# Optimization experiments

Hardware: AMD Instinct MI355X
Metric: run time of the kernel (lower is better)

The kernel has to match this reference:

```python
import jax, jax.numpy as jnp
import numpy as np

NUM_GRAPHS = 64
NEG_SLOPE = 0.1


def gcn_conv(x, src, dst, W, b, num_nodes):
    h = x @ W  # [N, out]
    ones = jnp.ones(src.shape[0], dtype=x.dtype)
    deg = jax.ops.segment_sum(ones, dst, num_segments=num_nodes) + 1.0  # +1 self-loop
    dinv = jax.lax.rsqrt(deg)  # deg >= 1 always
    coef = dinv[src] * dinv[dst]  # [E]
    agg = jax.ops.segment_sum(h[src] * coef[:, None], dst, num_segments=num_nodes)
    # self-loop contribution: dinv[i]^2 * h[i]
    out = agg + h * (dinv * dinv)[:, None] + b
    return out


def leaky_relu(x):
    return jnp.where(x >= 0, x, NEG_SLOPE * x)


def global_mean_pool(x, batch, num_graphs):
    s = jax.ops.segment_sum(x, batch, num_segments=num_graphs)
    cnt = jax.ops.segment_sum(jnp.ones(x.shape[0], dtype=x.dtype), batch, num_segments=num_graphs)
    return s / jnp.maximum(cnt, 1.0)[:, None]


def setup_inputs() -> dict:
    key = jax.random.key(0)
    ks = jax.random.split(key, 10)
    N, E, D_IN, D_H, D_OUT, C = 50000, 600000, 128, 128, 128, 16
    x = jax.random.normal(ks[0], (N, D_IN), dtype=jnp.float32)
    edge_index = jax.random.randint(ks[1], (2, E), 0, N, dtype=jnp.int32)
    batch = jnp.sort(jax.random.randint(ks[2], (N,), 0, NUM_GRAPHS, dtype=jnp.int32))
    def glorot(k, shape):
        lim = np.sqrt(6.0 / (shape[0] + shape[1]))
        return jax.random.uniform(k, shape, jnp.float32, -lim, lim)
    W1 = glorot(ks[3], (D_IN, D_H))
    b1 = jnp.zeros((D_H,), jnp.float32)
    W2 = glorot(ks[4], (D_H, D_OUT))
    b2 = jnp.zeros((D_OUT,), jnp.float32)
    Wl = glorot(ks[5], (D_OUT, C))
    bl = jnp.zeros((C,), jnp.float32)
    return {"x": x, "edge_index": edge_index, "batch": batch,
            "W1": W1, "b1": b1, "W2": W2, "b2": b2, "Wl": Wl, "bl": bl}


def reference(x, edge_index, batch, W1, b1, W2, b2, Wl, bl):
    N = x.shape[0]
    src, dst = edge_index[0], edge_index[1]
    h = gcn_conv(x, src, dst, W1, b1, N)
    h = leaky_relu(h)
    h = gcn_conv(h, src, dst, W2, b2, N)
    h = leaky_relu(h)
    g = global_mean_pool(h, batch, NUM_GRAPHS)  # [G, D_OUT]
    # dropout p=0.2 is identity in eval mode
    return g @ Wl + bl
```

## Files before the change

kernel.cpp:

```cpp
#include <hip/hip_runtime.h>

#define D 128
#define NG 64
#define NC 16
#define NEG 0.1f

typedef __attribute__((ext_vector_type(8))) short bf16x8;
typedef __attribute__((ext_vector_type(4))) float f32x4;

__device__ __forceinline__ float bf2f(unsigned int u16) {
    union { unsigned int i; float f; } c;
    c.i = u16 << 16;
    return c.f;
}
__device__ __forceinline__ unsigned short f2bf(float f) {
    union { float f; unsigned int i; } c;
    c.f = f;
    unsigned int i = c.i;
    unsigned int r = (i + 0x7FFFu + ((i >> 16) & 1u)) >> 16;
    return (unsigned short)r;
}

__global__ void prep_misc_kernel(const float* __restrict__ W1, unsigned short* __restrict__ Wf1,
                                 const float* __restrict__ W2, unsigned short* __restrict__ Wf2,
                                 float* __restrict__ pooled,
                                 const int* __restrict__ dst, int* __restrict__ deg, int E) {
    int b = blockIdx.x;
    if (b < 16) {
        const float* W = (b < 8) ? W1 : W2;
        unsigned short* Wf = (b < 8) ? Wf1 : Wf2;
        int fid = (b & 7) * 256 + threadIdx.x;
        int m = fid & 15;
        int quad = (fid >> 4) & 3;
        int kc = (fid >> 6) & 3;
        int t = fid >> 8;
        int n = t * 16 + m;
        int k0 = kc * 32 + quad * 8;
        unsigned short r[8];
#pragma unroll
        for (int j = 0; j < 8; j++) r[j] = f2bf(W[(k0 + j) * 128 + n]);
        uint4 v;
        v.x = (unsigned int)r[0] | ((unsigned int)r[1] << 16);
        v.y = (unsigned int)r[2] | ((unsigned int)r[3] << 16);
        v.z = (unsigned int)r[4] | ((unsigned int)r[5] << 16);
        v.w = (unsigned int)r[6] | ((unsigned int)r[7] << 16);
        ((uint4*)Wf)[fid] = v;
    } else if (b < 48) {
        pooled[(b - 16) * 256 + threadIdx.x] = 0.f;
    } else {
        int e = (b - 48) * 256 + threadIdx.x;
        if (e < E) atomicAdd(&deg[dst[e]], 1);
    }
}

__global__ void scan_block_kernel(const int* __restrict__ deg, int* __restrict__ scan1,
                                  int* __restrict__ blocksum, float* __restrict__ dinv, int N) {
    __shared__ int sm[256];
    int tid = threadIdx.x;
    int i = blockIdx.x * 256 + tid;
    int v = (i < N) ? deg[i] : 0;
    if (i < N) dinv[i] = 1.0f / sqrtf((float)v + 1.0f);
    sm[tid] = v;
    __syncthreads();
    for (int off = 1; off < 256; off <<= 1) {
        int t = (tid >= off) ? sm[tid - off] : 0;
        __syncthreads();
        sm[tid] += t;
        __syncthreads();
    }
    if (i < N) scan1[i] = sm[tid];
    if (tid == 255) blocksum[blockIdx.x] = sm[255];
}

__global__ void finalize_ptr_kernel(const int* __restrict__ deg, const int* __restrict__ scan1,
                                    const int* __restrict__ blocksum, int* __restrict__ ptr,
                                    int* __restrict__ fill, int nb, int N, int E) {
    __shared__ int sm[256];
    int tid = threadIdx.x;
    int v = (tid < nb) ? blocksum[tid] : 0;
    sm[tid] = v;
    __syncthreads();
    for (int off = 1; off < 256; off <<= 1) {
        int t = (tid >= off) ? sm[tid - off] : 0;
        __syncthreads();
        sm[tid] += t;
        __syncthreads();
    }
    int blockoff = (blockIdx.x > 0) ? sm[blockIdx.x - 1] : 0;
    int i = blockIdx.x * 256 + tid;
    if (i < N) {
        ptr[i] = scan1[i] - deg[i] + blockoff;
        fill[i] = 0;
        if (i == N - 1) ptr[N] = E;
    }
}

__global__ void scatter_kernel(const int* __restrict__ src, const int* __restrict__ dst,
                               const int* __restrict__ ptr, int* __restrict__ fill,
                               const float* __restrict__ dinv,
                               int2* __restrict__ csr_edge, int E) {
    int e = blockIdx.x * blockDim.x + threadIdx.x;
    if (e < E) {
        int d = dst[e];
        int s = src[e];
        int pos = ptr[d] + atomicAdd(&fill[d], 1);
        float coef = dinv[s] * dinv[d];
        csr_edge[pos] = make_int2(s, __float_as_int(coef));
    }
}

template <bool AF32>
__global__ __launch_bounds__(256) void gemm_mfma_kernel(const void* __restrict__ Ap,
                                                        const uint4* __restrict__ Wf,
                                                        unsigned int* __restrict__ C, int N) {
    __shared__ uint4 Ws[2048];
    int tid = threadIdx.x;
    int w = tid >> 6, lane = tid & 63;
    int quad = lane >> 4, m = lane & 15;
    int rowstart = blockIdx.x * 64;

#pragma unroll
    for (int i = 0; i < 8; i++) Ws[tid + 256 * i] = Wf[tid + 256 * i];

    int arow = rowstart + 16 * w + m;
    bool valid = arow < N;
    bf16x8 af[4];
    if (AF32) {
        const float* Ag = (const float*)Ap;
#pragma unroll
        for (int kc = 0; kc < 4; kc++) {
            float4 f0 = make_float4(0.f, 0.f, 0.f, 0.f), f1 = f0;
            if (valid) {
                const float4* p = (const float4*)(Ag + (size_t)arow * 128 + kc * 32 + quad * 8);
                f0 = p[0];
                f1 = p[1];
            }
            bf16x8 a;
            a[0] = (short)f2bf(f0.x); a[1] = (short)f2bf(f0.y);
            a[2] = (short)f2bf(f0.z); a[3] = (short)f2bf(f0.w);
            a[4] = (short)f2bf(f1.x); a[5] = (short)f2bf(f1.y);
            a[6] = (short)f2bf(f1.z); a[7] = (short)f2bf(f1.w);
            af[kc] = a;
        }
    } else {
        const unsigned short* Ag = (const unsigned short*)Ap;
#pragma unroll
        for (int kc = 0; kc < 4; kc++) {
            bf16x8 a;
#pragma unroll
            for (int j = 0; j < 8; j++) a[j] = 0;
            if (valid) a = *(const bf16x8*)(Ag + (size_t)arow * 128 + kc * 32 + quad * 8);
            af[kc] = a;
        }
    }
    __syncthreads();

    f32x4 acc[8];
#pragma unroll
    for (int t = 0; t < 8; t++) acc[t] = (f32x4){0.f, 0.f, 0.f, 0.f};

#pragma unroll
    for (int t = 0; t < 8; t++) {
#pragma unroll
        for (int kc = 0; kc < 4; kc++) {
            bf16x8 bh = *(const bf16x8*)&Ws[(((t * 4 + kc) * 4 + quad) * 16 + m)];
            acc[t] = __builtin_amdgcn_mfma_f32_16x16x32_bf16(af[kc], bh, acc[t], 0, 0, 0);
        }
    }

#pragma unroll
    for (int t = 0; t < 8; t++) {
#pragma unroll
        for (int r = 0; r < 4; r++) {
            int row = rowstart + 16 * w + quad * 4 + r;
            unsigned int us = f2bf(acc[t][r]);
            unsigned int other = (unsigned int)__shfl_xor((int)us, 1);
            if (((m & 1) == 0) && row < N)
                C[(size_t)row * 64 + t * 8 + (m >> 1)] = us | (other << 16);
        }
    }
}

__global__ void combine_kernel(const uint4* __restrict__ h4, const int* __restrict__ ptr,
                               const int2* __restrict__ csr_edge,
                               const float* __restrict__ dinv, const float* __restrict__ b,
                               uint4* __restrict__ out4, int N) {
    __shared__ int2 smeta[4][64];
    int wave = threadIdx.x >> 6;
    int lane = threadIdx.x & 63;
    int i = blockIdx.x * 4 + wave;
    if (i >= N) return;
    int q = lane >> 4;
    int l16 = lane & 15;

    int lo = ptr[i], hi = ptr[i + 1];
    int deg = hi - lo;

    float a0 = 0.f, a1 = 0.f, a2 = 0.f, a3 = 0.f, a4 = 0.f, a5 = 0.f, a6 = 0.f, a7 = 0.f;

    for (int base = 0; base < deg; base += 64) {
        int cnt = min(64, deg - base);
        if (lane < cnt) smeta[wave][lane] = csr_edge[lo + base + lane];
        int jj = q;
        for (; jj + 4 < cnt; jj += 8) {
            int2 e0 = smeta[wave][jj];
            int2 e1 = smeta[wave][jj + 4];
            float c0 = __int_as_float(e0.y);
            float c1 = __int_as_float(e1.y);
            uint4 v0 = h4[(size_t)e0.x * 16 + l16];
            uint4 v1 = h4[(size_t)e1.x * 16 + l16];
            a0 += bf2f(v0.x & 0xffffu) * c0; a1 += bf2f(v0.x >> 16) * c0;
            a2 += bf2f(v0.y & 0xffffu) * c0; a3 += bf2f(v0.y >> 16) * c0;
            a4 += bf2f(v0.z & 0xffffu) * c0; a5 += bf2f(v0.z >> 16) * c0;
            a6 += bf2f(v0.w & 0xffffu) * c0; a7 += bf2f(v0.w >> 16) * c0;
            a0 += bf2f(v1.x & 0xffffu) * c1; a1 += bf2f(v1.x >> 16) * c1;
            a2 += bf2f(v1.y & 0xffffu) * c1; a3 += bf2f(v1.y >> 16) * c1;
            a4 += bf2f(v1.z & 0xffffu) * c1; a5 += bf2f(v1.z >> 16) * c1;
            a6 += bf2f(v1.w & 0xffffu) * c1; a7 += bf2f(v1.w >> 16) * c1;
        }
        if (jj < cnt) {
            int2 e0 = smeta[wave][jj];
            float c0 = __int_as_float(e0.y);
            uint4 v0 = h4[(size_t)e0.x * 16 + l16];
            a0 += bf2f(v0.x & 0xffffu) * c0; a1 += bf2f(v0.x >> 16) * c0;
            a2 += bf2f(v0.y & 0xffffu) * c0; a3 += bf2f(v0.y >> 16) * c0;
            a4 += bf2f(v0.z & 0xffffu) * c0; a5 += bf2f(v0.z >> 16) * c0;
            a6 += bf2f(v0.w & 0xffffu) * c0; a7 += bf2f(v0.w >> 16) * c0;
        }
    }
    a0 += __shfl_xor(a0, 16); a0 += __shfl_xor(a0, 32);
    a1 += __shfl_xor(a1, 16); a1 += __shfl_xor(a1, 32);
    a2 += __shfl_xor(a2, 16); a2 += __shfl_xor(a2, 32);
    a3 += __shfl_xor(a3, 16); a3 += __shfl_xor(a3, 32);
    a4 += __shfl_xor(a4, 16); a4 += __shfl_xor(a4, 32);
    a5 += __shfl_xor(a5, 16); a5 += __shfl_xor(a5, 32);
    a6 += __shfl_xor(a6, 16); a6 += __shfl_xor(a6, 32);
    a7 += __shfl_xor(a7, 16); a7 += __shfl_xor(a7, 32);

    float di = dinv[i];
    uint4 sv = h4[(size_t)i * 16 + l16];
    float4 bv0 = ((const float4*)b)[l16 * 2];
    float4 bv1 = ((const float4*)b)[l16 * 2 + 1];
    float dd = di * di;
    float v0 = a0 + bf2f(sv.x & 0xffffu) * dd + bv0.x;
    float v1 = a1 + bf2f(sv.x >> 16) * dd + bv0.y;
    float v2 = a2 + bf2f(sv.y & 0xffffu) * dd + bv0.z;
    float v3 = a3 + bf2f(sv.y >> 16) * dd + bv0.w;
    float v4 = a4 + bf2f(sv.z & 0xffffu) * dd + bv1.x;
    float v5 = a5 + bf2f(sv.z >> 16) * dd + bv1.y;
    float v6 = a6 + bf2f(sv.w & 0xffffu) * dd + bv1.z;
    float v7 = a7 + bf2f(sv.w >> 16) * dd + bv1.w;
    v0 = (v0 >= 0.f) ? v0 : NEG * v0;
    v1 = (v1 >= 0.f) ? v1 : NEG * v1;
    v2 = (v2 >= 0.f) ? v2 : NEG * v2;
    v3 = (v3 >= 0.f) ? v3 : NEG * v3;
    v4 = (v4 >= 0.f) ? v4 : NEG * v4;
    v5 = (v5 >= 0.f) ? v5 : NEG * v5;
    v6 = (v6 >= 0.f) ? v6 : NEG * v6;
    v7 = (v7 >= 0.f) ? v7 : NEG * v7;
    if (q == 0) {
        uint4 pv;
        pv.x = (unsigned int)f2bf(v0) | ((unsigned int)f2bf(v1) << 16);
        pv.y = (unsigned int)f2bf(v2) | ((unsigned int)f2bf(v3) << 16);
        pv.z = (unsigned int)f2bf(v4) | ((unsigned int)f2bf(v5) << 16);
        pv.w = (unsigned int)f2bf(v6) | ((unsigned int)f2bf(v7) << 16);
        out4[(size_t)i * 16 + l16] = pv;
    }
}

#define PROWS 128
__global__ void pool_accum_kernel(const unsigned int* __restrict__ a2,
                                  const int* __restrict__ batch,
                                  float* __restrict__ pooled, int N) {
    int wave = threadIdx.x >> 6;
    int lane = threadIdx.x & 63;
    int start = blockIdx.x * PROWS;
    int end = start + PROWS;
    if (end > N) end = N;
    float s0 = 0.f, s1 = 0.f;
    int curg = -1;
    for (int r = start + wave; r < end; r += 4) {
        int g = batch[r];
        if (g != curg) {
            if (curg >= 0) {
                atomicAdd(&pooled[curg * D + 2 * lane], s0);
                atomicAdd(&pooled[curg * D + 2 * lane + 1], s1);
            }
            curg = g;
            s0 = 0.f;
            s1 = 0.f;
        }
        unsigned int v = a2[(size_t)r * 64 + lane];
        s0 += bf2f(v & 0xffffu);
        s1 += bf2f(v >> 16);
    }
    if (curg >= 0) {
        atomicAdd(&pooled[curg * D + 2 * lane], s0);
        atomicAdd(&pooled[curg * D + 2 * lane + 1], s1);
    }
}

__global__ void final_kernel(const float* __restrict__ pooled, const int* __restrict__ batch,
                             const float* __restrict__ Wl, const float* __restrict__ bl,
                             float* __restrict__ out, int N) {
    int t = blockIdx.x * blockDim.x + threadIdx.x;
    if (t >= NG * NC) return;
    int g = t >> 4, c = t & 15;
    int l = 0, h = N;
    while (l < h) { int m = (l + h) >> 1; if (batch[m] < g) l = m + 1; else h = m; }
    int lo = l;
    h = N;
    while (l < h) { int m = (l + h) >> 1; if (batch[m] < g + 1) l = m + 1; else h = m; }
    int cnt = l - lo;
    float inv = 1.0f / (float)(cnt > 0 ? cnt : 1);
    float dot = 0.f;
    for (int k = 0; k < D; k++) dot += pooled[g * D + k] * Wl[k * NC + c];
    out[t] = dot * inv + bl[c];
}

extern "C" void kernel_launch(void* const* d_in, const int* in_sizes, int n_in,
                              void* d_out, int out_size, void* d_ws, size_t ws_size,
                              hipStream_t stream) {
    const float* x = (const float*)d_in[0];
    const int* ei = (const int*)d_in[1];
    const int* batch = (const int*)d_in[2];
    const float* W1 = (const float*)d_in[3];
    const float* b1 = (const float*)d_in[4];
    const float* W2 = (const float*)d_in[5];
    const float* b2 = (const float*)d_in[6];
    const float* Wlin = (const float*)d_in[7];
    const float* bl = (const float*)d_in[8];
    float* out = (float*)d_out;

    int N = in_sizes[0] / D;
    int E = in_sizes[1] / 2;
    const int* src = ei;
    const int* dst = ei + E;

    float* ws = (float*)d_ws;
    size_t o = 0;
    unsigned int* bufA = (unsigned int*)(ws + o); o += (size_t)N * 64;
    unsigned int* bufB = (unsigned int*)(ws + o); o += (size_t)N * 64;
    int* deg = (int*)(ws + o);      o += N;
    int* fill = (int*)(ws + o);     o += N;
    float* dinv = ws + o;           o += N;
    int* scan1 = (int*)(ws + o);    o += N;
    int* blocksum = (int*)(ws + o); o += 256;
    int* csr_ptr = (int*)(ws + o);  o += (N + 4);
    int2* csr_edge = (int2*)(ws + o); o += (size_t)2 * E;
    float* pooled = ws + o;         o += NG * D;
    unsigned short* Wf1 = (unsigned short*)(ws + o); o += 8192;
    unsigned short* Wf2 = (unsigned short*)(ws + o); o += 8192;

    hipMemsetAsync(deg, 0, (size_t)N * sizeof(int), stream);

    int tb = 256;
    int nscan = (N + 255) / 256;
    prep_misc_kernel<<<48 + (E + 255) / 256, 256, 0, stream>>>(W1, Wf1, W2, Wf2, pooled,
                                                               dst, deg, E);
    scan_block_kernel<<<nscan, 256, 0, stream>>>(deg, scan1, blocksum, dinv, N);
    finalize_ptr_kernel<<<nscan, 256, 0, stream>>>(deg, scan1, blocksum, csr_ptr, fill,
                                                   nscan, N, E);
    scatter_kernel<<<(E + tb - 1) / tb, tb, 0, stream>>>(src, dst, csr_ptr, fill, dinv,
                                                         csr_edge, E);

    int gblocks = (N + 63) / 64;
    int cblocks = (N + 3) / 4;
    gemm_mfma_kernel<true><<<gblocks, 256, 0, stream>>>(x, (const uint4*)Wf1,
                                                        (unsigned int*)bufA, N);
    combine_kernel<<<cblocks, 256, 0, stream>>>((const uint4*)bufA, csr_ptr, csr_edge,
                                                dinv, b1, (uint4*)bufB, N);
    gemm_mfma_kernel<false><<<gblocks, 256, 0, stream>>>(bufB, (const uint4*)Wf2,
                                                         (unsigned int*)bufA, N);
    combine_kernel<<<cblocks, 256, 0, stream>>>((const uint4*)bufA, csr_ptr, csr_edge,
                                                dinv, b2, (uint4*)bufB, N);
    pool_accum_kernel<<<(N + PROWS - 1) / PROWS, 256, 0, stream>>>(bufB, batch, pooled, N);
    final_kernel<<<(NG * NC + tb - 1) / tb, tb, 0, stream>>>(pooled, batch, Wlin, bl, out, N);
}
```

Measured before the change: 251.7 us.

## Map one node per 16-lane quarter-wave in GCN combine kernel

The combine kernel now assigns four nodes per wave, one per 16-lane group, instead of one node per wave with its edges split across the four quarters. The cross-quarter shuffle reduction goes away, and the edge metadata for the wave's four-node range is staged jointly into shared memory. Each quarter loops over its own node's edges, with four gathers in flight per iteration, and the grid shrinks fourfold. Degree imbalance among the four nodes in a wave can now leave lanes idle, since quarters with short edge lists wait on the longest one.

Measured after the change: 243.6 us. 1.03x faster.

```diff
diff --git a/kernel.cpp b/kernel.cpp
--- a/kernel.cpp
+++ b/kernel.cpp
@@ -181,66 +181,77 @@
     }
 }
 
-__global__ void combine_kernel(const uint4* __restrict__ h4, const int* __restrict__ ptr,
-                               const int2* __restrict__ csr_edge,
-                               const float* __restrict__ dinv, const float* __restrict__ b,
-                               uint4* __restrict__ out4, int N) {
+#define ACC8(v, c)                                                         \
+    a0 += bf2f((v).x & 0xffffu) * (c); a1 += bf2f((v).x >> 16) * (c);      \
+    a2 += bf2f((v).y & 0xffffu) * (c); a3 += bf2f((v).y >> 16) * (c);      \
+    a4 += bf2f((v).z & 0xffffu) * (c); a5 += bf2f((v).z >> 16) * (c);      \
+    a6 += bf2f((v).w & 0xffffu) * (c); a7 += bf2f((v).w >> 16) * (c);
+
+__global__ __launch_bounds__(256) void combine_kernel(const uint4* __restrict__ h4,
+                                                      const int* __restrict__ ptr,
+                                                      const int2* __restrict__ csr_edge,
+                                                      const float* __restrict__ dinv,
+                                                      const float* __restrict__ b,
+                                                      uint4* __restrict__ out4, int N) {
     __shared__ int2 smeta[4][64];
     int wave = threadIdx.x >> 6;
     int lane = threadIdx.x & 63;
-    int i = blockIdx.x * 4 + wave;
-    if (i >= N) return;
     int q = lane >> 4;
     int l16 = lane & 15;
-
-    int lo = ptr[i], hi = ptr[i + 1];
-    int deg = hi - lo;
+    int nb = blockIdx.x * 16 + wave * 4;
+    if (nb >= N) return;
+    int node = nb + q;
+    bool valid = node < N;
+
+    int wlo = ptr[nb];
+    int whi = ptr[min(nb + 4, N)];
+    int lo = valid ? ptr[node] : 0;
+    int hi = valid ? ptr[node + 1] : 0;
+
+    float di = valid ? dinv[node] : 0.f;
+    uint4 sv = valid ? h4[(size_t)node * 16 + l16] : make_uint4(0u, 0u, 0u, 0u);
+    float4 bv0 = ((const float4*)b)[l16 * 2];
+    float4 bv1 = ((const float4*)b)[l16 * 2 + 1];
 
     float a0 = 0.f, a1 = 0.f, a2 = 0.f, a3 = 0.f, a4 = 0.f, a5 = 0.f, a6 = 0.f, a7 = 0.f;
 
-    for (int base = 0; base < deg; base += 64) {
-        int cnt = min(64, deg - base);
-        if (lane < cnt) smeta[wave][lane] = csr_edge[lo + base + lane];
-        int jj = q;
-        for (; jj + 4 < cnt; jj += 8) {
-            int2 e0 = smeta[wave][jj];
-            int2 e1 = smeta[wave][jj + 4];
+#pragma unroll 1
+    for (int base = wlo; base < whi; base += 64) {
+        if (base + lane < whi) smeta[wave][lane] = csr_edge[base + lane];
+        int s = max(lo, base);
+        int e = min(hi, base + 64);
+        int j = s;
+#pragma unroll 1
+        for (; j + 3 < e; j += 4) {
+            int k = j - base;
+            int2 e0 = smeta[wave][k];
+            int2 e1 = smeta[wave][k + 1];
+            int2 e2 = smeta[wave][k + 2];
+            int2 e3 = smeta[wave][k + 3];
+            uint4 v0 = h4[(size_t)e0.x * 16 + l16];
+            uint4 v1 = h4[(size_t)e1.x * 16 + l16];
+            uint4 v2 = h4[(size_t)e2.x * 16 + l16];
+            uint4 v3 = h4[(size_t)e3.x * 16 + l16];
             float c0 = __int_as_float(e0.y);
             float c1 = __int_as_float(e1.y);
+            float c2 = __int_as_float(e2.y);
+            float c3 = __int_as_float(e3.y);
+            ACC8(v0, c0)
+            ACC8(v1, c1)
+            ACC8(v2, c2)
+            ACC8(v3, c3)
+        }
+#pragma unroll 1
+        for (; j < e; j++) {
+            int k = j - base;
+            int2 e0 = smeta[wave][k];
             uint4 v0 = h4[(size_t)e0.x * 16 + l16];
-            uint4 v1 = h4[(size_t)e1.x * 16 + l16];
-            a0 += bf2f(v0.x & 0xffffu) * c0; a1 += bf2f(v0.x >> 16) * c0;
-            a2 += bf2f(v0.y & 0xffffu) * c0; a3 += bf2f(v0.y >> 16) * c0;
-            a4 += bf2f(v0.z & 0xffffu) * c0; a5 += bf2f(v0.z >> 16) * c0;
-            a6 += bf2f(v0.w & 0xffffu) * c0; a7 += bf2f(v0.w >> 16) * c0;
-            a0 += bf2f(v1.x & 0xffffu) * c1; a1 += bf2f(v1.x >> 16) * c1;
-            a2 += bf2f(v1.y & 0xffffu) * c1; a3 += bf2f(v1.y >> 16) * c1;
-            a4 += bf2f(v1.z & 0xffffu) * c1; a5 += bf2f(v1.z >> 16) * c1;
-            a6 += bf2f(v1.w & 0xffffu) * c1; a7 += bf2f(v1.w >> 16) * c1;
-        }
-        if (jj < cnt) {
-            int2 e0 = smeta[wave][jj];
             float c0 = __int_as_float(e0.y);
-            uint4 v0 = h4[(size_t)e0.x * 16 + l16];
-            a0 += bf2f(v0.x & 0xffffu) * c0; a1 += bf2f(v0.x >> 16) * c0;
-            a2 += bf2f(v0.y & 0xffffu) * c0; a3 += bf2f(v0.y >> 16) * c0;
-            a4 += bf2f(v0.z & 0xffffu) * c0; a5 += bf2f(v0.z >> 16) * c0;
-            a6 += bf2f(v0.w & 0xffffu) * c0; a7 += bf2f(v0.w >> 16) * c0;
-        }
-    }
-    a0 += __shfl_xor(a0, 16); a0 += __shfl_xor(a0, 32);
-    a1 += __shfl_xor(a1, 16); a1 += __shfl_xor(a1, 32);
-    a2 += __shfl_xor(a2, 16); a2 += __shfl_xor(a2, 32);
-    a3 += __shfl_xor(a3, 16); a3 += __shfl_xor(a3, 32);
-    a4 += __shfl_xor(a4, 16); a4 += __shfl_xor(a4, 32);
-    a5 += __shfl_xor(a5, 16); a5 += __shfl_xor(a5, 32);
-    a6 += __shfl_xor(a6, 16); a6 += __shfl_xor(a6, 32);
-    a7 += __shfl_xor(a7, 16); a7 += __shfl_xor(a7, 32);
-
-    float di = dinv[i];
-    uint4 sv = h4[(size_t)i * 16 + l16];
-    float4 bv0 = ((const float4*)b)[l16 * 2];
-    float4 bv1 = ((const float4*)b)[l16 * 2 + 1];
+            ACC8(v0, c0)
+        }
+    }
+
+    if (!valid) return;
     float dd = di * di;
     float v0 = a0 + bf2f(sv.x & 0xffffu) * dd + bv0.x;
     float v1 = a1 + bf2f(sv.x >> 16) * dd + bv0.y;
@@ -258,14 +269,12 @@
     v5 = (v5 >= 0.f) ? v5 : NEG * v5;
     v6 = (v6 >= 0.f) ? v6 : NEG * v6;
     v7 = (v7 >= 0.f) ? v7 : NEG * v7;
-    if (q == 0) {
-        uint4 pv;
-        pv.x = (unsigned int)f2bf(v0) | ((unsigned int)f2bf(v1) << 16);
-        pv.y = (unsigned int)f2bf(v2) | ((unsigned int)f2bf(v3) << 16);
-        pv.z = (unsigned int)f2bf(v4) | ((unsigned int)f2bf(v5) << 16);
-        pv.w = (unsigned int)f2bf(v6) | ((unsigned int)f2bf(v7) << 16);
-        out4[(size_t)i * 16 + l16] = pv;
-    }
+    uint4 pv;
+    pv.x = (unsigned int)f2bf(v0) | ((unsigned int)f2bf(v1) << 16);
+    pv.y = (unsigned int)f2bf(v2) | ((unsigned int)f2bf(v3) << 16);
+    pv.z = (unsigned int)f2bf(v4) | ((unsigned int)f2bf(v5) << 16);
+    pv.w = (unsigned int)f2bf(v6) | ((unsigned int)f2bf(v7) << 16);
+    out4[(size_t)node * 16 + l16] = pv;
 }
 
 #define PROWS 128
@@ -365,7 +374,7 @@
                                                          csr_edge, E);
 
     int gblocks = (N + 63) / 64;
-    int cblocks = (N + 3) / 4;
+    int cblocks = (N + 15) / 16;
     gemm_mfma_kernel<true><<<gblocks, 256, 0, stream>>>(x, (const uint4*)Wf1,
                                                         (unsigned int*)bufA, N);
     combine_kernel<<<cblocks, 256, 0, stream>>>((const uint4*)bufA, csr_ptr, csr_edge,
```
